# Optimization experiments

Hardware: AMD Instinct MI355X
Metric: run time of the kernel (lower is better)

The kernel has to match this reference:

```python
import jax, jax.numpy as jnp
import numpy as np

HID = 1024; NH = 4; HD = HID // NH; KS = 4; C = 64; EPS = 1e-05
B = 4; L = 4096


def setup_inputs():
    key = jax.random.key(0)
    ks = jax.random.split(key, 9)
    return {
        "x": jax.random.normal(ks[0], (B, L, HID), jnp.float32),
        "Wq": jax.random.normal(ks[1], (HID, HID), jnp.float32) * 0.02,
        "Wk": jax.random.normal(ks[2], (HID, HID), jnp.float32) * 0.02,
        "Wv": jax.random.normal(ks[3], (HID, HID), jnp.float32) * 0.02,
        "Wb": jax.random.normal(ks[4], (HID, NH), jnp.float32) * 0.02,
        "conv_q": jax.random.normal(ks[5], (HID, 1, KS), jnp.float32) * 0.5,
        "conv_k": jax.random.normal(ks[6], (HID, 1, KS), jnp.float32) * 0.5,
        "conv_v": jax.random.normal(ks[7], (HID, 1, KS), jnp.float32) * 0.5,
        "g": jnp.ones((HD,), jnp.float32),
        "Wo": jax.random.normal(ks[8], (HID, HID), jnp.float32) * 0.02,
    }


def _causal_dwconv(x, w):
    # x: (B, L, Ch); w: (Ch, 1, K). Depthwise causal conv (left pad K-1) + SiLU,
    # equivalent to torch Conv1d(padding=K-1) followed by right-truncation.
    xc = jnp.moveaxis(x, 1, 2)  # (B, Ch, L)
    y = jax.lax.conv_general_dilated(
        xc, w, window_strides=(1,), padding=[(w.shape[-1] - 1, 0)],
        dimension_numbers=("NCH", "OIH", "NCH"), feature_group_count=w.shape[0])
    return jnp.moveaxis(jax.nn.silu(y), 1, 2)


def _forward(x, Wq, Wk, Wv, Wb, conv_q, conv_k, conv_v, g, Wo):
    Bx, Lx, _ = x.shape
    N = Lx // C  # num chunks (L chosen divisible by C)
    q = _causal_dwconv(x @ Wq, conv_q).reshape(Bx, Lx, NH, HD)
    k = _causal_dwconv(x @ Wk, conv_k).reshape(Bx, Lx, NH, HD)
    v = _causal_dwconv(x @ Wv, conv_v).reshape(Bx, Lx, NH, HD)
    # kq_norm: L2-normalize each head vector over head_dim
    q = q / jnp.linalg.norm(q, axis=-1, keepdims=True)
    k = k / jnp.linalg.norm(k, axis=-1, keepdims=True)
    beta = jax.nn.sigmoid(x @ Wb)  # (B, L, H)
    Q = q.reshape(Bx, N, C, NH, HD)
    K = k.reshape(Bx, N, C, NH, HD)
    V = v.reshape(Bx, N, C, NH, HD)
    bta = beta.reshape(Bx, N, C, NH, 1)
    Kb = K * bta
    Vb = V * bta
    # T = eye(C) - sum_h tril(Kb_h @ K_h^T, -1)  (T shared across heads, as in source)
    A = jnp.einsum("bnihd,bnjhd->bnij", Kb, K)
    T0 = jnp.eye(C, dtype=x.dtype) - jnp.tril(A, -1)
    col = jnp.arange(C)

    def body(i, T):
        # Replicates: T[:,:,i,:i] += (T[:,:,i,:,None] * T[:,:,:,:i]).sum(-2)
        row = jax.lax.dynamic_slice_in_dim(T, i, 1, axis=2)[:, :, 0]  # (B,N,C)
        acc = jnp.einsum("bnj,bnjc->bnc", row, T)
        new_row = jnp.where(col < i, row + acc, row)
        return jax.lax.dynamic_update_slice_in_dim(T, new_row[:, :, None, :], i, axis=2)

    T = jax.lax.fori_loop(1, C, body, T0)
    W = jnp.einsum("bnij,bnjhd->bnihd", T, Kb)
    U = jnp.einsum("bnij,bnjhd->bnihd", T, Vb)

    def chunk_step(S, inp):
        q_i, k_i, w_i, u0 = inp  # each (B, C, H, D)
        # source einsum 'bchd,bhdd->bchd' extracts the diagonal of S
        Sd = jnp.diagonal(S, axis1=-2, axis2=-1)  # (B, H, D)
        u_i = u0 - w_i * Sd[:, None]
        o_inter = q_i * Sd[:, None]
        # source: einsum('bchd,bchd->bc', q, k).tril() -- tril over the (B, C) matrix
        A_i = jnp.tril(jnp.einsum("bchd,bchd->bc", q_i, k_i))
        o_intra = A_i[:, :, None, None] * u_i
        S = S + jnp.einsum("bchd,bche->bhde", k_i, u_i)
        return S, o_inter + o_intra

    xs = tuple(jnp.moveaxis(a, 1, 0) for a in (Q, K, W, U))  # (N, B, C, H, D)
    S0 = jnp.zeros((Bx, NH, HD, HD), x.dtype)
    S, O = jax.lax.scan(chunk_step, S0, xs)
    o = jnp.moveaxis(O, 0, 1).reshape(Bx, Lx, NH, HD)
    # RMSNorm over head_dim with learned scale g
    o = o * jax.lax.rsqrt(jnp.mean(o * o, axis=-1, keepdims=True) + EPS) * g
    out = o.reshape(Bx, Lx, NH * HD) @ Wo
    return out, S


def reference(x, Wq, Wk, Wv, Wb, conv_q, conv_k, conv_v, g, Wo):
    return _forward(x, Wq, Wk, Wv, Wb, conv_q, conv_k, conv_v, g, Wo)
```

## Files before the change

### kernel.cpp

```cpp
#include <hip/hip_runtime.h>
#include <hip/hip_bf16.h>

#define HID 1024
#define NH 4
#define HD 256
#define NCH 64
#define BB 4
#define LL 4096
#define ROWS (BB*LL)
#define SSIZE (BB*NH*HD*HD)

typedef __hip_bfloat16 bf16;
typedef __attribute__((ext_vector_type(8))) short short8;
typedef __attribute__((ext_vector_type(4))) float f32x4;

struct u16x4 { unsigned short x, y, z, w; };

__device__ __forceinline__ float bfu2f(unsigned short u) {
  return __uint_as_float(((unsigned int)u) << 16);
}
__device__ __forceinline__ unsigned short f2bfu(float f) {
  unsigned int x = __float_as_uint(f);
  return (unsigned short)((x + 0x7FFFu + ((x >> 16) & 1u)) >> 16);
}
__device__ __forceinline__ float ldv(const float* p) { return *p; }
__device__ __forceinline__ float ldv(const bf16* p) { return bfu2f(*(const unsigned short*)p); }
__device__ __forceinline__ float4 ld4(const float* p) { return *(const float4*)p; }
__device__ __forceinline__ float4 ld4(const bf16* p) {
  u16x4 u = *(const u16x4*)p;
  return make_float4(bfu2f(u.x), bfu2f(u.y), bfu2f(u.z), bfu2f(u.w));
}
__device__ __forceinline__ void st4(float* p, float4 v) { *(float4*)p = v; }
__device__ __forceinline__ void st4(bf16* p, float4 v) {
  u16x4 u; u.x = f2bfu(v.x); u.y = f2bfu(v.y); u.z = f2bfu(v.z); u.w = f2bfu(v.w);
  *(u16x4*)p = u;
}
__device__ __forceinline__ void stc(float* C, size_t i, float v) { C[i] = v; }
__device__ __forceinline__ void stc(bf16* C, size_t i, float v) {
  ((unsigned short*)C)[i] = f2bfu(v);
}

typedef const __attribute__((address_space(1))) unsigned int* gptr_t;
typedef __attribute__((address_space(3))) unsigned int* lptr_t;
__device__ __forceinline__ void gload16(const void* g, void* l) {
  __builtin_amdgcn_global_load_lds((gptr_t)g, (lptr_t)l, 16, 0, 0);
}


template <typename OT>
__device__ __forceinline__
void gemm_body(const unsigned short* __restrict__ A,
               const unsigned short* __restrict__ Bt, OT* __restrict__ C,
               int m0, int n0, unsigned short* Asl, unsigned short* Bsl) {
  const int tid = threadIdx.x;
  const int wave = tid >> 6, lane = tid & 63;
  const int wr = wave >> 1, wc = wave & 1;
  f32x4 acc[4][4] = {};
  const int cA = (wave << 6) + lane;
  for (int k0 = 0; k0 < HID; k0 += 32) {
#pragma unroll
    for (int i = 0; i < 2; ++i) {
      int c = cA + (i << 8);
      int row = c >> 2, ko = (c & 3) << 3;
      gload16(&A[(size_t)(m0 + row) * HID + k0 + ko],
              &Asl[(size_t)((i << 8) + (wave << 6)) * 8]);
      gload16(&Bt[(size_t)(n0 + row) * HID + k0 + ko],
              &Bsl[(size_t)((i << 8) + (wave << 6)) * 8]);
    }
    __syncthreads();
    short8 af[4], bfr[4];
#pragma unroll
    for (int f = 0; f < 4; ++f) {
      int ra = (wr << 6) + (f << 4) + (lane & 15);
      af[f] = *(const short8*)&Asl[ra * 32 + ((lane >> 4) << 3)];
      int rb = (wc << 6) + (f << 4) + (lane & 15);
      bfr[f] = *(const short8*)&Bsl[rb * 32 + ((lane >> 4) << 3)];
    }
#pragma unroll
    for (int i = 0; i < 4; ++i)
#pragma unroll
      for (int j = 0; j < 4; ++j)
        acc[i][j] = __builtin_amdgcn_mfma_f32_16x16x32_bf16(af[i], bfr[j],
                                                            acc[i][j], 0, 0, 0);
    __syncthreads();
  }
#pragma unroll
  for (int i = 0; i < 4; ++i) {
    int r0 = m0 + (wr << 6) + (i << 4) + ((lane >> 4) << 2);
#pragma unroll
    for (int j = 0; j < 4; ++j) {
      int c0 = n0 + (wc << 6) + (j << 4) + (lane & 15);
#pragma unroll
      for (int r = 0; r < 4; ++r)
        stc(C, (size_t)(r0 + r) * HID + c0, acc[i][j][r]);
    }
  }
}

template <int MODE, typename IT, typename ST>
__device__ __forceinline__
void conv8_body(const IT* __restrict__ lin, const float* __restrict__ w,
                const float* __restrict__ beta, ST* __restrict__ out, int row0) {
  const int tid = threadIdx.x;
  const int ch = tid << 2;
  const int h = tid >> 6;
  float wv[4][4];
#pragma unroll
  for (int j = 0; j < 4; ++j) {
    float4 t4 = *(const float4*)&w[(ch + j) << 2];
    wv[j][0] = t4.x; wv[j][1] = t4.y; wv[j][2] = t4.z; wv[j][3] = t4.w;
  }
  const int l0 = row0 & (LL - 1);
  const bool hasprev = (l0 != 0);
  float4 xw0, xw1, xw2, xw3;
  const float4 z4 = make_float4(0.f, 0.f, 0.f, 0.f);
  xw0 = hasprev ? ld4(&lin[(size_t)(row0 - 3) * HID + ch]) : z4;
  xw1 = hasprev ? ld4(&lin[(size_t)(row0 - 2) * HID + ch]) : z4;
  xw2 = hasprev ? ld4(&lin[(size_t)(row0 - 1) * HID + ch]) : z4;
#pragma unroll
  for (int r = 0; r < 8; ++r) {
    const int gr = row0 + r;
    xw3 = ld4(&lin[(size_t)gr * HID + ch]);
    float y[4];
#pragma unroll
    for (int j = 0; j < 4; ++j) {
      float xv0 = j == 0 ? xw0.x : j == 1 ? xw0.y : j == 2 ? xw0.z : xw0.w;
      float xv1 = j == 0 ? xw1.x : j == 1 ? xw1.y : j == 2 ? xw1.z : xw1.w;
      float xv2 = j == 0 ? xw2.x : j == 1 ? xw2.y : j == 2 ? xw2.z : xw2.w;
      float xv3 = j == 0 ? xw3.x : j == 1 ? xw3.y : j == 2 ? xw3.z : xw3.w;
      y[j] = xv0 * wv[j][0] + xv1 * wv[j][1] + xv2 * wv[j][2] + xv3 * wv[j][3];
      y[j] = y[j] / (1.f + expf(-y[j]));
    }
    float scale;
    if (MODE < 2) {
      float ss = y[0]*y[0] + y[1]*y[1] + y[2]*y[2] + y[3]*y[3];
#pragma unroll
      for (int off = 32; off; off >>= 1) ss += __shfl_xor(ss, off);
      scale = 1.f / sqrtf(ss);
    } else {
      scale = beta[(gr << 2) + h];
    }
    st4(&out[(size_t)gr * HID + ch],
        make_float4(y[0]*scale, y[1]*scale, y[2]*scale, y[3]*scale));
    xw0 = xw1; xw1 = xw2; xw2 = xw3;
  }
}


__global__ __launch_bounds__(256)
void prep_convT(const float* __restrict__ x, const float* __restrict__ Wb,
                const float* __restrict__ Wq, const float* __restrict__ Wv,
                const float* __restrict__ Wo, const float* __restrict__ Wk,
                bf16* __restrict__ hi, bf16* __restrict__ lo,
                float* __restrict__ beta,
                unsigned short* __restrict__ Wqt, unsigned short* __restrict__ Wvt,
                unsigned short* __restrict__ Wot, unsigned short* __restrict__ Wkht,
                unsigned short* __restrict__ Wklt) {
  __shared__ float t[64][65];
  const int bx = blockIdx.x;
  const int tid = threadIdx.x;
  if (bx < 4096) {
    const int wave = tid >> 6, lane = tid & 63;
    const int m = (bx << 2) + wave;
    float a0 = 0.f, a1 = 0.f, a2 = 0.f, a3 = 0.f;
#pragma unroll
    for (int it = 0; it < 4; ++it) {
      int f4 = (it << 6) + lane;
      size_t e = (size_t)m * 256 + f4;
      float4 v = *(const float4*)&x[e << 2];
      u16x4 h; h.x = f2bfu(v.x); h.y = f2bfu(v.y); h.z = f2bfu(v.z); h.w = f2bfu(v.w);
      *(u16x4*)&hi[e << 2] = h;
      u16x4 l;
      l.x = f2bfu(v.x - bfu2f(h.x)); l.y = f2bfu(v.y - bfu2f(h.y));
      l.z = f2bfu(v.z - bfu2f(h.z)); l.w = f2bfu(v.w - bfu2f(h.w));
      *(u16x4*)&lo[e << 2] = l;
      const float xs[4] = {v.x, v.y, v.z, v.w};
#pragma unroll
      for (int j = 0; j < 4; ++j) {
        float4 wb = *(const float4*)&Wb[((f4 << 2) + j) << 2];
        a0 += xs[j] * wb.x; a1 += xs[j] * wb.y;
        a2 += xs[j] * wb.z; a3 += xs[j] * wb.w;
      }
    }
#pragma unroll
    for (int off = 32; off; off >>= 1) {
      a0 += __shfl_xor(a0, off); a1 += __shfl_xor(a1, off);
      a2 += __shfl_xor(a2, off); a3 += __shfl_xor(a3, off);
    }
    if (lane == 0) {
      float4 r;
      r.x = 1.f / (1.f + expf(-a0)); r.y = 1.f / (1.f + expf(-a1));
      r.z = 1.f / (1.f + expf(-a2)); r.w = 1.f / (1.f + expf(-a3));
      *(float4*)&beta[m << 2] = r;
    }
  } else {
    const int idx = bx - 4096;
    const int z = idx >> 8;
    const int xy = idx & 255;
    const int kt = (xy & 15) << 6, nt = (xy >> 4) << 6;
    const float* W = z == 0 ? Wq : z == 1 ? Wv : z == 2 ? Wo : Wk;
#pragma unroll
    for (int i = 0; i < 16; ++i) {
      int id2 = tid + (i << 8);
      int r = id2 >> 6, c = id2 & 63;
      t[r][c] = W[(size_t)(kt + r) * HID + nt + c];
    }
    __syncthreads();
    if (z < 3) {
      unsigned short* Wt = z == 0 ? Wqt : z == 1 ? Wvt : Wot;
#pragma unroll
      for (int i = 0; i < 16; ++i) {
        int id2 = tid + (i << 8);
        int n = id2 >> 6, kk = id2 & 63;
        Wt[(size_t)(nt + n) * HID + kt + kk] = f2bfu(t[kk][n]);
      }
    } else {
#pragma unroll
      for (int i = 0; i < 16; ++i) {
        int id2 = tid + (i << 8);
        int n = id2 >> 6, kk = id2 & 63;
        float v = t[kk][n];
        unsigned short h = f2bfu(v);
        Wkht[(size_t)(nt + n) * HID + kt + kk] = h;
        Wklt[(size_t)(nt + n) * HID + kt + kk] = f2bfu(v - bfu2f(h));
      }
    }
  }
}

__global__ __launch_bounds__(256)
void mfma_gemm3(const unsigned short* __restrict__ Ah_,
                const unsigned short* __restrict__ Al_,
                const unsigned short* __restrict__ Bh_,
                const unsigned short* __restrict__ Bl_,
                float* __restrict__ C) {
  __shared__ unsigned short Ah[128 * 32];
  __shared__ unsigned short Al[128 * 32];
  __shared__ unsigned short Bh[128 * 32];
  __shared__ unsigned short Bl[128 * 32];
  const int tid = threadIdx.x;
  const int wave = tid >> 6, lane = tid & 63;
  const int m0 = blockIdx.x << 7, n0 = blockIdx.y << 7;
  const int wr = wave >> 1, wc = wave & 1;
  f32x4 acc[4][4] = {};
  const int cA = (wave << 6) + lane;
  for (int k0 = 0; k0 < HID; k0 += 32) {
#pragma unroll
    for (int i = 0; i < 2; ++i) {
      int c = cA + (i << 8);
      int row = c >> 2, ko = (c & 3) << 3;
      size_t ga = (size_t)(m0 + row) * HID + k0 + ko;
      size_t gb = (size_t)(n0 + row) * HID + k0 + ko;
      size_t ldst = (size_t)((i << 8) + (wave << 6)) * 8;
      gload16(&Ah_[ga], &Ah[ldst]);
      gload16(&Al_[ga], &Al[ldst]);
      gload16(&Bh_[gb], &Bh[ldst]);
      gload16(&Bl_[gb], &Bl[ldst]);
    }
    __syncthreads();
    short8 ah[4], al[4], bh[4], bl[4];
#pragma unroll
    for (int f = 0; f < 4; ++f) {
      int ra = ((wr << 6) + (f << 4) + (lane & 15)) * 32 + ((lane >> 4) << 3);
      ah[f] = *(const short8*)&Ah[ra];
      al[f] = *(const short8*)&Al[ra];
      int rb = ((wc << 6) + (f << 4) + (lane & 15)) * 32 + ((lane >> 4) << 3);
      bh[f] = *(const short8*)&Bh[rb];
      bl[f] = *(const short8*)&Bl[rb];
    }
#pragma unroll
    for (int i = 0; i < 4; ++i)
#pragma unroll
      for (int j = 0; j < 4; ++j) {
        f32x4 a = acc[i][j];
        a = __builtin_amdgcn_mfma_f32_16x16x32_bf16(al[i], bh[j], a, 0, 0, 0);
        a = __builtin_amdgcn_mfma_f32_16x16x32_bf16(ah[i], bl[j], a, 0, 0, 0);
        a = __builtin_amdgcn_mfma_f32_16x16x32_bf16(ah[i], bh[j], a, 0, 0, 0);
        acc[i][j] = a;
      }
    __syncthreads();
  }
#pragma unroll
  for (int i = 0; i < 4; ++i) {
    int r0 = m0 + (wr << 6) + (i << 4) + ((lane >> 4) << 2);
#pragma unroll
    for (int j = 0; j < 4; ++j) {
      int c0 = n0 + (wc << 6) + (j << 4) + (lane & 15);
#pragma unroll
      for (int r = 0; r < 4; ++r)
        C[(size_t)(r0 + r) * HID + c0] = acc[i][j][r];
    }
  }
}

__global__ __launch_bounds__(256)
void conv8_k(const float* __restrict__ lin, const float* __restrict__ w,
             const float* __restrict__ beta, float* __restrict__ out) {
  conv8_body<1, float, float>(lin, w, beta, out, blockIdx.x << 3);
}

__global__ __launch_bounds__(256)
void qv_gemm(const unsigned short* __restrict__ A,
             const unsigned short* __restrict__ Wqt,
             const unsigned short* __restrict__ Wvt,
             bf16* __restrict__ linq, bf16* __restrict__ linv) {
  __shared__ unsigned short Asl[128 * 32];
  __shared__ unsigned short Bsl[128 * 32];
  const unsigned short* Bt = blockIdx.z ? Wvt : Wqt;
  bf16* C = blockIdx.z ? linv : linq;
  gemm_body<bf16>(A, Bt, C, blockIdx.x << 7, blockIdx.y << 7, Asl, Bsl);
}

__global__ __launch_bounds__(256)
void convqv_ktrans(const bf16* __restrict__ linq, const bf16* __restrict__ linv,
                   const float* __restrict__ cq, const float* __restrict__ cv,
                   const float* __restrict__ beta, bf16* __restrict__ qbuf,
                   bf16* __restrict__ vbuf, const float* __restrict__ k,
                   unsigned short* __restrict__ kt) {
  __shared__ float t[64][65];
  const int bx = blockIdx.x;
  if (bx < 2048) {
    conv8_body<0, bf16, bf16>(linq, cq, beta, qbuf, bx << 3);
  } else if (bx < 4096) {
    conv8_body<2, bf16, bf16>(linv, cv, beta, vbuf, (bx - 2048) << 3);
  } else {
    const int idx = bx - 4096;
    const int r0 = (idx & 255) << 6, c0 = (idx >> 8) << 6;
    const int tid = threadIdx.x;
#pragma unroll
    for (int i = 0; i < 16; ++i) {
      int id2 = tid + (i << 8);
      int rr = id2 >> 6, cc = id2 & 63;
      t[rr][cc] = k[(size_t)(r0 + rr) * HID + c0 + cc];
    }
    __syncthreads();
#pragma unroll
    for (int i = 0; i < 16; ++i) {
      int id2 = tid + (i << 8);
      int cc = id2 >> 6, rr = id2 & 63;
      kt[(size_t)(c0 + cc) * ROWS + r0 + rr] = f2bfu(t[rr][cc]);
    }
  }
}

__global__ __launch_bounds__(256)
void chunkT_kernel(const float* __restrict__ k, const float* __restrict__ beta,
                   float* __restrict__ Tg) {
  __shared__ float T[64][68];
  __shared__ float S1[64][68];
  __shared__ float S2[64][68];
  __shared__ float row_s[64];
  const int bn = blockIdx.x;
  const size_t base = (size_t)bn * 64 * HID;
  const int tid = threadIdx.x;
  const int tr = tid >> 4, tc = tid & 15;
  float acc[4][4] = {{0.f}};
  for (int d0 = 0; d0 < HID; d0 += 64) {
    const int h = d0 >> 8;
#pragma unroll
    for (int p = 0; p < 4; ++p) {
      int rr = (tid >> 4) + (p << 4);
      int c4 = (tid & 15) << 2;
      float4 a = *(const float4*)&k[base + (size_t)rr * HID + d0 + c4];
      float bta = beta[(((bn << 6) + rr) << 2) + h];
      S2[c4 + 0][rr] = a.x; S2[c4 + 1][rr] = a.y;
      S2[c4 + 2][rr] = a.z; S2[c4 + 3][rr] = a.w;
      S1[c4 + 0][rr] = a.x * bta; S1[c4 + 1][rr] = a.y * bta;
      S1[c4 + 2][rr] = a.z * bta; S1[c4 + 3][rr] = a.w * bta;
    }
    __syncthreads();
#pragma unroll
    for (int dd = 0; dd < 64; ++dd) {
      float4 a = *(const float4*)&S1[dd][tr << 2];
      float4 b = *(const float4*)&S2[dd][tc << 2];
      acc[0][0] += a.x*b.x; acc[0][1] += a.x*b.y; acc[0][2] += a.x*b.z; acc[0][3] += a.x*b.w;
      acc[1][0] += a.y*b.x; acc[1][1] += a.y*b.y; acc[1][2] += a.y*b.z; acc[1][3] += a.y*b.w;
      acc[2][0] += a.z*b.x; acc[2][1] += a.z*b.y; acc[2][2] += a.z*b.z; acc[2][3] += a.z*b.w;
      acc[3][0] += a.w*b.x; acc[3][1] += a.w*b.y; acc[3][2] += a.w*b.z; acc[3][3] += a.w*b.w;
    }
    __syncthreads();
  }
#pragma unroll
  for (int i = 0; i < 4; ++i)
#pragma unroll
    for (int j = 0; j < 4; ++j) {
      int ri = (tr << 2) + i, cj = (tc << 2) + j;
      T[ri][cj] = (ri == cj) ? 1.f : (ri > cj ? -acc[i][j] : 0.f);
    }
  __syncthreads();
  for (int i = 1; i < 64; ++i) {
    if (tid < 64) row_s[tid] = T[i][tid];
    __syncthreads();
    if (tid < 64) {
      float a = 0.f;
#pragma unroll 8
      for (int j = 0; j < 64; ++j) a += row_s[j] * T[j][tid];
      if (tid < i) T[i][tid] = row_s[tid] + a;
    }
    __syncthreads();
  }
#pragma unroll
  for (int ii = 0; ii < 4; ++ii) {
    int off = (tid << 4) + (ii << 2);
    int c = off >> 6, j = off & 63;
    *(float4*)&Tg[(size_t)bn * 4096 + off] = *(const float4*)&T[c][j];
  }
}

__global__ __launch_bounds__(256)
void prct_kernel(const float* __restrict__ k, const bf16* __restrict__ v,
                 const float* __restrict__ beta, const float* __restrict__ Tg,
                 float* __restrict__ P, float* __restrict__ R) {
  __shared__ float Ts[4096];
  __shared__ float bs[64];
  const int bn = blockIdx.x >> 2, h = blockIdx.x & 3;
  const int tid = threadIdx.x;
#pragma unroll
  for (int ii = 0; ii < 4; ++ii) {
    int off = (tid << 4) + (ii << 2);
    *(float4*)&Ts[off] = *(const float4*)&Tg[(size_t)bn * 4096 + off];
  }
  if (tid < 64) bs[tid] = beta[(((bn << 6) + tid) << 2) + h];
  __syncthreads();
  const int ch = (h << 8) + tid;
  const size_t base = (size_t)bn * 64 * HID;
  float ct[64];
#pragma unroll
  for (int j = 0; j < 64; ++j) ct[j] = 0.f;
  for (int c = 0; c < 64; ++c) {
    float kc = k[base + (size_t)c * HID + ch];
#pragma unroll
    for (int j = 0; j < 64; ++j) ct[j] += Ts[(c << 6) + j] * kc;
  }
  float p = 0.f, r = 0.f;
#pragma unroll
  for (int j = 0; j < 64; ++j) {
    float kj = k[base + (size_t)j * HID + ch];
    float vj = ldv(&v[base + (size_t)j * HID + ch]);
    p += bs[j] * kj * ct[j];
    r += vj * ct[j];
  }
  P[(size_t)bn * HID + ch] = p;
  R[(size_t)bn * HID + ch] = r;
}

__global__ __launch_bounds__(256)
void scan_ai(const float* __restrict__ P, const float* __restrict__ R,
             float* __restrict__ Sdp, const bf16* __restrict__ q,
             const float* __restrict__ k, float* __restrict__ Ai) {
  const int bx = blockIdx.x;
  if (bx < 16) {
    const int b = bx >> 2;
    const int ch = ((bx & 3) << 8) + threadIdx.x;
    float S = 0.f;
    float p = P[(size_t)(b << 6) * HID + ch];
    float r = R[(size_t)(b << 6) * HID + ch];
    for (int n = 0; n < 64; ++n) {
      Sdp[(size_t)((n << 2) + b) * HID + ch] = S;
      float pn = 0.f, rn = 0.f;
      if (n < 63) {
        pn = P[(size_t)((b << 6) + n + 1) * HID + ch];
        rn = R[(size_t)((b << 6) + n + 1) * HID + ch];
      }
      S = S * (1.f - p) + r;
      p = pn; r = rn;
    }
  } else {
    const int bn = bx - 16;
    const int b = bn >> 6;
    const int wave = threadIdx.x >> 6, lane = threadIdx.x & 63;
    const size_t roff = ((size_t)bn * 64 + wave) * HID;
    float s = 0.f;
#pragma unroll
    for (int it = 0; it < 4; ++it) {
      int d = (lane << 2) + (it << 8);
      float4 a = ld4(&q[roff + d]);
      float4 b4 = *(const float4*)&k[roff + d];
      s += a.x*b4.x + a.y*b4.y + a.z*b4.z + a.w*b4.w;
    }
#pragma unroll
    for (int off = 32; off; off >>= 1) s += __shfl_xor(s, off);
    if (lane == 0) Ai[(bn << 2) + wave] = (wave <= b) ? s : 0.f;
  }
}

__global__ __launch_bounds__(256)
void ucompute_kernel(const float* __restrict__ k, const bf16* __restrict__ v,
                     const float* __restrict__ beta, const float* __restrict__ Tg,
                     const float* __restrict__ Sdp, unsigned short* __restrict__ Ut) {
  __shared__ float Ts[4096];
  __shared__ float va[64][132];
  __shared__ float bs[64];
  const int bn = blockIdx.x >> 3;
  const int rr2 = blockIdx.x & 7;
  const int h = rr2 >> 1, eh = rr2 & 1;
  const int b = bn >> 6, nl = bn & 63;
  const int tid = threadIdx.x;
#pragma unroll
  for (int ii = 0; ii < 4; ++ii) {
    int off = (tid << 4) + (ii << 2);
    *(float4*)&Ts[off] = *(const float4*)&Tg[(size_t)bn * 4096 + off];
  }
  if (tid < 64) bs[tid] = beta[(((bn << 6) + tid) << 2) + h];
  __syncthreads();
  const size_t base = (size_t)bn * 64 * HID;
  const int ch0 = (h << 8) + (eh << 7);
#pragma unroll
  for (int p = 0; p < 8; ++p) {
    int idx = tid + (p << 8);
    int row = idx >> 5;
    int col4 = (idx & 31) << 2;
    int chg = ch0 + col4;
    float4 sd4 = *(const float4*)&Sdp[(size_t)((nl << 2) + b) * HID + chg];
    float4 k4 = *(const float4*)&k[base + (size_t)row * HID + chg];
    float4 v4 = ld4(&v[base + (size_t)row * HID + chg]);
    float bt = bs[row];
    va[row][col4 + 0] = v4.x - bt * k4.x * sd4.x;
    va[row][col4 + 1] = v4.y - bt * k4.y * sd4.y;
    va[row][col4 + 2] = v4.z - bt * k4.z * sd4.z;
    va[row][col4 + 3] = v4.w - bt * k4.w * sd4.w;
  }
  __syncthreads();
  const int e = tid & 127;
  const int chalf = tid >> 7;
  float acc[32];
#pragma unroll
  for (int c2 = 0; c2 < 32; ++c2) acc[c2] = 0.f;
  for (int j = 0; j < 64; ++j) {
    float vaj = va[j][e];
#pragma unroll
    for (int c2 = 0; c2 < 32; ++c2)
      acc[c2] += Ts[((chalf << 5) + c2) * 64 + j] * vaj;
  }
  const size_t ub = ((size_t)(((b << 2) + h) * HD) + (eh << 7) + e) * LL
                  + (nl << 6) + (chalf << 5);
#pragma unroll
  for (int c4 = 0; c4 < 8; ++c4) {
    u16x4 u;
    u.x = f2bfu(acc[(c4 << 2) + 0]); u.y = f2bfu(acc[(c4 << 2) + 1]);
    u.z = f2bfu(acc[(c4 << 2) + 2]); u.w = f2bfu(acc[(c4 << 2) + 3]);
    *(u16x4*)&Ut[ub + (c4 << 2)] = u;
  }
}

__global__ __launch_bounds__(256)
void o_gemmS(bf16* __restrict__ q, const float* __restrict__ Sdp,
             const unsigned short* __restrict__ Ut, const float* __restrict__ Ai,
             const float* __restrict__ g, const unsigned short* __restrict__ At,
             float* __restrict__ Spart, int ngroups) {
  __shared__ unsigned short Asl[128 * 32];
  __shared__ unsigned short Bsl[128 * 32];
  const int bx = blockIdx.x;
  const int tid = threadIdx.x;
  if (bx < 16384) {
    const int row = bx;
    const int b = row >> 12;
    const int l = row & (LL - 1);
    const int n = l >> 6, c = l & 63;
    const int ch = tid << 2;
    const size_t ro = (size_t)row * HID;
    float4 qv = ld4(&q[ro + ch]);
    float4 sd = *(const float4*)&Sdp[(size_t)((n << 2) + b) * HID + ch];
    float ox = qv.x*sd.x, oy = qv.y*sd.y, oz = qv.z*sd.z, ow = qv.w*sd.w;
    if (c <= b) {
      int bn = (b << 6) + n;
      float a = Ai[(bn << 2) + c];
      const int h = ch >> 8, e = ch & 255;
      const size_t ub = ((size_t)(((b << 2) + h) * HD) + e) * LL + (n << 6) + c;
      ox += a * bfu2f(Ut[ub + 0 * LL]);
      oy += a * bfu2f(Ut[ub + 1 * LL]);
      oz += a * bfu2f(Ut[ub + 2 * LL]);
      ow += a * bfu2f(Ut[ub + 3 * LL]);
    }
    float ss = ox*ox + oy*oy + oz*oz + ow*ow;
#pragma unroll
    for (int off = 32; off; off >>= 1) ss += __shfl_xor(ss, off);
    float scale = 1.f / sqrtf(ss * (1.f / HD) + 1e-5f);
    float4 gv = *(const float4*)&g[ch & (HD - 1)];
    st4(&q[ro + ch], make_float4(ox*scale*gv.x, oy*scale*gv.y, oz*scale*gv.z, ow*scale*gv.w));
  } else {
    const int zz = bx - 16384;
    const int m0 = (zz & 1) << 7, n0 = ((zz >> 1) & 1) << 7;
    const int zidx = zz >> 2;
    const int bh = zidx / ngroups;
    const int ng = zidx % ngroups;
    const int b = bh >> 2, h = bh & 3;
    const size_t kbase = (size_t)b * LL + (size_t)ng * (LL / ngroups);
    const int wave = tid >> 6, lane = tid & 63;
    const int wr = wave >> 1, wc = wave & 1;
    f32x4 acc[4][4] = {};
    const int cA = (wave << 6) + lane;
    for (int k0 = 0; k0 < LL / ngroups; k0 += 32) {
#pragma unroll
      for (int i = 0; i < 2; ++i) {
        int c = cA + (i << 8);
        int row = c >> 2, ko = (c & 3) << 3;
        gload16(&At[((size_t)(h * HD + m0 + row)) * ROWS + kbase + k0 + ko],
                &Asl[(size_t)((i << 8) + (wave << 6)) * 8]);
        gload16(&Ut[((size_t)(bh * HD + n0 + row)) * LL + (size_t)ng * (LL / ngroups) + k0 + ko],
                &Bsl[(size_t)((i << 8) + (wave << 6)) * 8]);
      }
      __syncthreads();
      short8 af[4], bfr[4];
#pragma unroll
      for (int f = 0; f < 4; ++f) {
        int ra = (wr << 6) + (f << 4) + (lane & 15);
        af[f] = *(const short8*)&Asl[ra * 32 + ((lane >> 4) << 3)];
        int rb = (wc << 6) + (f << 4) + (lane & 15);
        bfr[f] = *(const short8*)&Bsl[rb * 32 + ((lane >> 4) << 3)];
      }
#pragma unroll
      for (int i = 0; i < 4; ++i)
#pragma unroll
        for (int j = 0; j < 4; ++j)
          acc[i][j] = __builtin_amdgcn_mfma_f32_16x16x32_bf16(af[i], bfr[j],
                                                              acc[i][j], 0, 0, 0);
      __syncthreads();
    }
    float* Cp = Spart + (size_t)ng * SSIZE + (size_t)bh * HD * HD;
#pragma unroll
    for (int i = 0; i < 4; ++i) {
      int r0 = m0 + (wr << 6) + (i << 4) + ((lane >> 4) << 2);
#pragma unroll
      for (int j = 0; j < 4; ++j) {
        int c0 = n0 + (wc << 6) + (j << 4) + (lane & 15);
#pragma unroll
        for (int r = 0; r < 4; ++r)
          Cp[(size_t)(r0 + r) * HD + c0] = acc[i][j][r];
      }
    }
  }
}

__global__ __launch_bounds__(256)
void out_sreduce(const unsigned short* __restrict__ A,
                 const unsigned short* __restrict__ Bt, float* __restrict__ C,
                 const float* __restrict__ Spart, float* __restrict__ Sout,
                 int ngroups) {
  __shared__ unsigned short Asl[128 * 32];
  __shared__ unsigned short Bsl[128 * 32];
  const int bx = blockIdx.x;
  if (bx < 1024) {
    gemm_body<float>(A, Bt, C, (bx >> 3) << 7, (bx & 7) << 7, Asl, Bsl);
  } else {
    size_t i = ((size_t)(bx - 1024) * 256 + threadIdx.x) << 2;
    float4 s = make_float4(0.f, 0.f, 0.f, 0.f);
    for (int g = 0; g < ngroups; ++g) {
      float4 p = *(const float4*)&Spart[(size_t)g * SSIZE + i];
      s.x += p.x; s.y += p.y; s.z += p.z; s.w += p.w;
    }
    *(float4*)&Sout[i] = s;
  }
}

extern "C" void kernel_launch(void* const* d_in, const int* in_sizes, int n_in,
                              void* d_out, int out_size, void* d_ws, size_t ws_size,
                              hipStream_t stream) {
  const float* x  = (const float*)d_in[0];
  const float* Wq = (const float*)d_in[1];
  const float* Wk = (const float*)d_in[2];
  const float* Wv = (const float*)d_in[3];
  const float* Wb = (const float*)d_in[4];
  const float* cq = (const float*)d_in[5];
  const float* ck = (const float*)d_in[6];
  const float* cv = (const float*)d_in[7];
  const float* g  = (const float*)d_in[8];
  const float* Wo = (const float*)d_in[9];
  float* out  = (float*)d_out;
  float* Sout = out + (size_t)ROWS * HID;

  const size_t F = (size_t)ROWS * HID;
  char* w = (char*)d_ws;
  float* kbuf  = (float*)w;  w += F * 4;
  bf16*  xb    = (bf16*)w;   w += F * 2;
  bf16*  qbuf  = (bf16*)w;   w += F * 2;
  bf16*  vbuf  = (bf16*)w;   w += F * 2;
  unsigned short* Wqt  = (unsigned short*)w; w += (size_t)HID * HID * 2;
  unsigned short* Wvt  = (unsigned short*)w; w += (size_t)HID * HID * 2;
  unsigned short* Wot  = (unsigned short*)w; w += (size_t)HID * HID * 2;
  unsigned short* Wkht = (unsigned short*)w; w += (size_t)HID * HID * 2;
  unsigned short* Wklt = (unsigned short*)w; w += (size_t)HID * HID * 2;
  float* Tg    = (float*)w;  w += (size_t)BB * NCH * 4096 * 4;
  float* betab = (float*)w;  w += (size_t)ROWS * NH * 4;
  float* Aib   = (float*)w;  w += (size_t)BB * NCH * 4 * 4;
  float* Pb    = (float*)w;  w += (size_t)BB * NCH * HID * 4;
  float* Rb    = (float*)w;  w += (size_t)BB * NCH * HID * 4;
  float* Sdp   = (float*)w;  w += (size_t)BB * NCH * HID * 4;
  const size_t need = (size_t)(w - (char*)d_ws);
  if (ws_size < need) return;

  dim3 gg(ROWS / 128, HID / 128);
  float* linf = out;
  bf16*  linq = (bf16*)out;
  bf16*  linv = linq + F;
  bf16*  xlo  = qbuf;

  prep_convT<<<4096 + 1024, 256, 0, stream>>>(x, Wb, Wq, Wv, Wo, Wk, xb, xlo,
                                              betab, Wqt, Wvt, Wot, Wkht, Wklt);
  mfma_gemm3<<<gg, 256, 0, stream>>>((const unsigned short*)xb,
                                     (const unsigned short*)xlo, Wkht, Wklt, linf);
  conv8_k<<<ROWS / 8, 256, 0, stream>>>(linf, ck, betab, kbuf);
  qv_gemm<<<dim3(ROWS / 128, HID / 128, 2), 256, 0, stream>>>(
      (const unsigned short*)xb, Wqt, Wvt, linq, linv);
  unsigned short* kt = (unsigned short*)xb;
  convqv_ktrans<<<2048 + 2048 + 4096, 256, 0, stream>>>(linq, linv, cq, cv,
                                                        betab, qbuf, vbuf,
                                                        kbuf, kt);
  chunkT_kernel<<<BB * NCH, 256, 0, stream>>>(kbuf, betab, Tg);
  prct_kernel<<<BB * NCH * NH, 256, 0, stream>>>(kbuf, vbuf, betab, Tg, Pb, Rb);
  scan_ai<<<16 + BB * NCH, 256, 0, stream>>>(Pb, Rb, Sdp, qbuf, kbuf, Aib);
  unsigned short* Ut = (unsigned short*)out;
  ucompute_kernel<<<BB * NCH * NH * 2, 256, 0, stream>>>(kbuf, vbuf, betab, Tg,
                                                         Sdp, Ut);
  float* Spart = kbuf;
  const int ngroups = 8;
  o_gemmS<<<16384 + 512, 256, 0, stream>>>(qbuf, Sdp, Ut, Aib, g, kt, Spart,
                                           ngroups);
  out_sreduce<<<1024 + SSIZE / 1024, 256, 0, stream>>>(
      (const unsigned short*)qbuf, Wot, out, Spart, Sout, ngroups);
}
```

Before: 685.1 us.

## Use double-buffered 256x256 tile GEMM for QV and output projections

Adds a 512-thread GEMM body with 256x256 output tiles, double-buffered LDS, and global-to-LDS loads for the next K step overlapped with MFMA work. It also raises wave priority around the MFMAs. The QV projection and output projection now use this kernel, and the S partial reduction moves to its own launch. Larger tiles improve operand reuse and the prefetch hides load latency, at the cost of fewer blocks (256–512) on a large-CU device, higher register use, and one extra kernel launch.

```diff
diff --git a/kernel.cpp b/kernel.cpp
--- a/kernel.cpp
+++ b/kernel.cpp
@@ -45,6 +45,9 @@
 __device__ __forceinline__ void gload16(const void* g, void* l) {
   __builtin_amdgcn_global_load_lds((gptr_t)g, (lptr_t)l, 16, 0, 0);
 }
+
+#define MEMFENCE asm volatile("" ::: "memory")
+#define RAWBAR() do { MEMFENCE; __builtin_amdgcn_s_barrier(); MEMFENCE; } while (0)
 
 
 template <typename OT>
@@ -87,6 +90,85 @@
 #pragma unroll
   for (int i = 0; i < 4; ++i) {
     int r0 = m0 + (wr << 6) + (i << 4) + ((lane >> 4) << 2);
+#pragma unroll
+    for (int j = 0; j < 4; ++j) {
+      int c0 = n0 + (wc << 6) + (j << 4) + (lane & 15);
+#pragma unroll
+      for (int r = 0; r < 4; ++r)
+        stc(C, (size_t)(r0 + r) * HID + c0, acc[i][j][r]);
+    }
+  }
+}
+
+template <typename OT>
+__device__ __forceinline__
+void gemm256_body(const unsigned short* __restrict__ A,
+                  const unsigned short* __restrict__ Bt, OT* __restrict__ C,
+                  int m0, int n0, unsigned short (*As)[256][32],
+                  unsigned short (*Bs)[256][32]) {
+  const int tid = threadIdx.x;
+  const int w = tid >> 6, lane = tid & 63;
+  const int wr = w >> 2, wc = w & 3;
+  const int srow = (lane >> 2);
+  const int scol = (lane & 3) << 3;
+  const int frow = lane & 15;
+  const int fk = (lane >> 4) << 3;
+  f32x4 acc[8][4] = {};
+  const int NT = HID / 32;
+
+#pragma unroll
+  for (int ii = 0; ii < 2; ++ii) {
+    gload16(&A[(size_t)(m0 + (ii << 7) + (w << 4) + srow) * HID + scol],
+            &As[0][(ii << 7) + (w << 4)][0]);
+    gload16(&Bt[(size_t)(n0 + (ii << 7) + (w << 4) + srow) * HID + scol],
+            &Bs[0][(ii << 7) + (w << 4)][0]);
+  }
+  asm volatile("s_waitcnt vmcnt(0)" ::: "memory");
+  RAWBAR();
+
+  for (int t = 0; t < NT; ++t) {
+    const int s = t & 1;
+    const int kn = (t + 1) << 5;
+    const bool more = (t + 1 < NT);
+#pragma unroll
+    for (int p = 0; p < 4; ++p) {
+      const int mh = p >> 1, nh = p & 1;
+      short8 af[4], bf2[2];
+#pragma unroll
+      for (int i2 = 0; i2 < 4; ++i2)
+        af[i2] = *(const short8*)&As[s][(wr << 7) + ((mh * 4 + i2) << 4) + frow][fk];
+#pragma unroll
+      for (int j2 = 0; j2 < 2; ++j2)
+        bf2[j2] = *(const short8*)&Bs[s][(wc << 6) + ((nh * 2 + j2) << 4) + frow][fk];
+      if (more) {
+        if (p < 2)
+          gload16(&A[(size_t)(m0 + (p << 7) + (w << 4) + srow) * HID + kn + scol],
+                  &As[s ^ 1][(p << 7) + (w << 4)][0]);
+        else
+          gload16(&Bt[(size_t)(n0 + ((p - 2) << 7) + (w << 4) + srow) * HID + kn + scol],
+                  &Bs[s ^ 1][((p - 2) << 7) + (w << 4)][0]);
+      }
+      RAWBAR();
+      __builtin_amdgcn_s_setprio(1);
+#pragma unroll
+      for (int i2 = 0; i2 < 4; ++i2)
+#pragma unroll
+        for (int j2 = 0; j2 < 2; ++j2)
+          acc[mh * 4 + i2][nh * 2 + j2] =
+              __builtin_amdgcn_mfma_f32_16x16x32_bf16(
+                  af[i2], bf2[j2], acc[mh * 4 + i2][nh * 2 + j2], 0, 0, 0);
+      __builtin_amdgcn_s_setprio(0);
+      if (p < 3) {
+        RAWBAR();
+      } else {
+        asm volatile("s_waitcnt vmcnt(0)" ::: "memory");
+        RAWBAR();
+      }
+    }
+  }
+#pragma unroll
+  for (int i = 0; i < 8; ++i) {
+    int r0 = m0 + (wr << 7) + (i << 4) + ((lane >> 4) << 2);
 #pragma unroll
     for (int j = 0; j < 4; ++j) {
       int c0 = n0 + (wc << 6) + (j << 4) + (lane & 15);
@@ -299,16 +381,28 @@
   conv8_body<1, float, float>(lin, w, beta, out, blockIdx.x << 3);
 }
 
-__global__ __launch_bounds__(256)
-void qv_gemm(const unsigned short* __restrict__ A,
-             const unsigned short* __restrict__ Wqt,
-             const unsigned short* __restrict__ Wvt,
-             bf16* __restrict__ linq, bf16* __restrict__ linv) {
-  __shared__ unsigned short Asl[128 * 32];
-  __shared__ unsigned short Bsl[128 * 32];
-  const unsigned short* Bt = blockIdx.z ? Wvt : Wqt;
-  bf16* C = blockIdx.z ? linv : linq;
-  gemm_body<bf16>(A, Bt, C, blockIdx.x << 7, blockIdx.y << 7, Asl, Bsl);
+__global__ __launch_bounds__(512)
+void qv_gemm256(const unsigned short* __restrict__ A,
+                const unsigned short* __restrict__ Wqt,
+                const unsigned short* __restrict__ Wvt,
+                bf16* __restrict__ linq, bf16* __restrict__ linv) {
+  __shared__ unsigned short As[2][256][32];
+  __shared__ unsigned short Bs[2][256][32];
+  const int bx = blockIdx.x;
+  const int z = bx >> 8;
+  const int ti = bx & 255;
+  const unsigned short* Bt = z ? Wvt : Wqt;
+  bf16* C = z ? linv : linq;
+  gemm256_body<bf16>(A, Bt, C, (ti >> 2) << 8, (ti & 3) << 8, As, Bs);
+}
+
+__global__ __launch_bounds__(512)
+void out_gemm256(const unsigned short* __restrict__ A,
+                 const unsigned short* __restrict__ Bt, float* __restrict__ C) {
+  __shared__ unsigned short As[2][256][32];
+  __shared__ unsigned short Bs[2][256][32];
+  gemm256_body<float>(A, Bt, C, (blockIdx.x >> 2) << 8, (blockIdx.x & 3) << 8,
+                      As, Bs);
 }
 
 __global__ __launch_bounds__(256)
@@ -633,24 +727,15 @@
 }
 
 __global__ __launch_bounds__(256)
-void out_sreduce(const unsigned short* __restrict__ A,
-                 const unsigned short* __restrict__ Bt, float* __restrict__ C,
-                 const float* __restrict__ Spart, float* __restrict__ Sout,
-                 int ngroups) {
-  __shared__ unsigned short Asl[128 * 32];
-  __shared__ unsigned short Bsl[128 * 32];
-  const int bx = blockIdx.x;
-  if (bx < 1024) {
-    gemm_body<float>(A, Bt, C, (bx >> 3) << 7, (bx & 7) << 7, Asl, Bsl);
-  } else {
-    size_t i = ((size_t)(bx - 1024) * 256 + threadIdx.x) << 2;
-    float4 s = make_float4(0.f, 0.f, 0.f, 0.f);
-    for (int g = 0; g < ngroups; ++g) {
-      float4 p = *(const float4*)&Spart[(size_t)g * SSIZE + i];
-      s.x += p.x; s.y += p.y; s.z += p.z; s.w += p.w;
-    }
-    *(float4*)&Sout[i] = s;
-  }
+void sreduce_kernel(const float* __restrict__ Spart, float* __restrict__ Sout,
+                    int ngroups) {
+  size_t i = ((size_t)blockIdx.x * 256 + threadIdx.x) << 2;
+  float4 s = make_float4(0.f, 0.f, 0.f, 0.f);
+  for (int g = 0; g < ngroups; ++g) {
+    float4 p = *(const float4*)&Spart[(size_t)g * SSIZE + i];
+    s.x += p.x; s.y += p.y; s.z += p.z; s.w += p.w;
+  }
+  *(float4*)&Sout[i] = s;
 }
 
 extern "C" void kernel_launch(void* const* d_in, const int* in_sizes, int n_in,
@@ -700,8 +785,8 @@
   mfma_gemm3<<<gg, 256, 0, stream>>>((const unsigned short*)xb,
                                      (const unsigned short*)xlo, Wkht, Wklt, linf);
   conv8_k<<<ROWS / 8, 256, 0, stream>>>(linf, ck, betab, kbuf);
-  qv_gemm<<<dim3(ROWS / 128, HID / 128, 2), 256, 0, stream>>>(
-      (const unsigned short*)xb, Wqt, Wvt, linq, linv);
+  qv_gemm256<<<512, 512, 0, stream>>>((const unsigned short*)xb, Wqt, Wvt,
+                                      linq, linv);
   unsigned short* kt = (unsigned short*)xb;
   convqv_ktrans<<<2048 + 2048 + 4096, 256, 0, stream>>>(linq, linv, cq, cv,
                                                         betab, qbuf, vbuf,
@@ -716,6 +801,6 @@
   const int ngroups = 8;
   o_gemmS<<<16384 + 512, 256, 0, stream>>>(qbuf, Sdp, Ut, Aib, g, kt, Spart,
                                            ngroups);
-  out_sreduce<<<1024 + SSIZE / 1024, 256, 0, stream>>>(
-      (const unsigned short*)qbuf, Wot, out, Spart, Sout, ngroups);
-}
+  out_gemm256<<<256, 512, 0, stream>>>((const unsigned short*)qbuf, Wot, out);
+  sreduce_kernel<<<SSIZE / 1024, 256, 0, stream>>>(Spart, Sout, ngroups);
+}
```

Measured after the change: 705.1 us. 1.03x slower.
